# Kernel optimization log

Measured on AMD Instinct MI355X. Metric: run time of the kernel, lower is better.

Reference implementation:

```python
import jax, jax.numpy as jnp
import numpy as np

EMBED = 1024
HEADS = 16
HEAD_DIM = EMBED // HEADS


def setup_inputs() -> dict:
    key = jax.random.key(0)
    ks = jax.random.split(key, 9)
    B, S = 1, 4096
    scale = 1.0 / np.sqrt(EMBED)
    x = jax.random.normal(ks[0], (B, S, EMBED), dtype=jnp.float32)
    # nn.Linear weights stored as [out, in]; we store transposed [in, out] for x @ W
    Wq = jax.random.uniform(ks[1], (EMBED, EMBED), jnp.float32, -scale, scale)
    bq = jax.random.uniform(ks[2], (EMBED,), jnp.float32, -scale, scale)
    Wk = jax.random.uniform(ks[3], (EMBED, EMBED), jnp.float32, -scale, scale)
    bk = jax.random.uniform(ks[4], (EMBED,), jnp.float32, -scale, scale)
    Wv = jax.random.uniform(ks[5], (EMBED, EMBED), jnp.float32, -scale, scale)
    bv = jax.random.uniform(ks[6], (EMBED,), jnp.float32, -scale, scale)
    Wo = jax.random.uniform(ks[7], (EMBED, EMBED), jnp.float32, -scale, scale)
    bo = jax.random.uniform(ks[8], (EMBED,), jnp.float32, -scale, scale)
    return {"x": x, "Wq": Wq, "bq": bq, "Wk": Wk, "bk": bk,
            "Wv": Wv, "bv": bv, "Wo": Wo, "bo": bo}


def reference(x, Wq, bq, Wk, bk, Wv, bv, Wo, bo):
    B, S, E = x.shape
    H, D = HEADS, HEAD_DIM
    # projections
    Q = (x @ Wq + bq).reshape(B, S, H, D).transpose(0, 2, 1, 3)  # [B,H,S,D]
    K = (x @ Wk + bk).reshape(B, S, H, D).transpose(0, 2, 1, 3)
    V = (x @ Wv + bv).reshape(B, S, H, D).transpose(0, 2, 1, 3)
    # unfused attention: full [B,H,S,S] score matrix, matching the torch module
    scores = jnp.einsum('bhqd,bhkd->bhqk', Q, K) / jnp.sqrt(jnp.float32(D)).astype(x.dtype)
    probs = jax.nn.softmax(scores, axis=-1)
    out = jnp.einsum('bhqk,bhkd->bhqd', probs, V)  # [B,H,S,D]
    out = out.transpose(0, 2, 1, 3).reshape(B, S, E)
    return out @ Wo + bo
```

## Files before the change

### kernel.cpp

```cpp
#include <hip/hip_runtime.h>


constexpr int Sq = 4096;
constexpr int Ee = 1024;
constexpr int Hh = 16;
constexpr int Dh = 64;

typedef _Float16 half8 __attribute__((ext_vector_type(8)));
typedef _Float16 half4 __attribute__((ext_vector_type(4)));
typedef _Float16 half2t __attribute__((ext_vector_type(2)));
typedef float f32x4 __attribute__((ext_vector_type(4)));

union U8 { half8 v8; half2t h2[4]; };

__device__ __forceinline__ unsigned short f2h(float f) {
  _Float16 h = (_Float16)f;
  return *reinterpret_cast<unsigned short*>(&h);
}

__device__ __forceinline__ half2t pk(float a, float b) {
  return __builtin_bit_cast(half2t, __builtin_amdgcn_cvt_pkrtz(a, b));
}

__device__ __forceinline__ void gload16(const void* g, void* l) {
  __builtin_amdgcn_global_load_lds(
      (const __attribute__((address_space(1))) void*)g,
      (__attribute__((address_space(3))) void*)l, 16, 0, 0);
}

__global__ void k_prep(const float* __restrict__ x,
                       const float* __restrict__ Wq, const float* __restrict__ Wk,
                       const float* __restrict__ Wv, const float* __restrict__ Wo,
                       unsigned short* __restrict__ xb,
                       unsigned short* __restrict__ Wqt, unsigned short* __restrict__ Wkt,
                       unsigned short* __restrict__ Wvt, unsigned short* __restrict__ Wot) {
  int b = blockIdx.x, t = threadIdx.x;
  if (b < 4096) {
    int i = b * 256 + t;
    float4 v = reinterpret_cast<const float4*>(x)[i];
    ushort4 o;
    o.x = f2h(v.x); o.y = f2h(v.y); o.z = f2h(v.z); o.w = f2h(v.w);
    reinterpret_cast<ushort4*>(xb)[i] = o;
    return;
  }
  __shared__ unsigned short tile[64][65];
  int r = b - 4096;
  int wi = r >> 8, ti = r & 255;
  const float* W = (wi == 0) ? Wq : (wi == 1) ? Wk : (wi == 2) ? Wv : Wo;
  unsigned short* Wt = (wi == 0) ? Wqt : (wi == 1) ? Wkt : (wi == 2) ? Wvt : Wot;
  int kb = (ti & 15) * 64, nb = (ti >> 4) * 64;
  int r0 = t >> 4, c4 = (t & 15) * 4;
  for (int i = 0; i < 4; i++) {
    int row = r0 + i * 16;
    float4 v = *reinterpret_cast<const float4*>(W + (size_t)(kb + row) * Ee + nb + c4);
    tile[row][c4 + 0] = f2h(v.x); tile[row][c4 + 1] = f2h(v.y);
    tile[row][c4 + 2] = f2h(v.z); tile[row][c4 + 3] = f2h(v.w);
  }
  __syncthreads();
  for (int i = 0; i < 4; i++) {
    int nrow = r0 + i * 16;
    ushort4 o;
    o.x = tile[c4 + 0][nrow]; o.y = tile[c4 + 1][nrow];
    o.z = tile[c4 + 2][nrow]; o.w = tile[c4 + 3][nrow];
    *reinterpret_cast<ushort4*>(Wt + (size_t)(nb + nrow) * Ee + kb + c4) = o;
  }
}

template <bool TR>
__device__ __forceinline__ void gemm_kloop(
    const unsigned short* __restrict__ A, const unsigned short* __restrict__ Wt,
    unsigned short* Al, unsigned short* Bl,
    int m0, int n0, int t, int wm, int wn, int quad, int c, f32x4 (&acc)[4][4]) {
  for (int k0 = 0; k0 < 1024; k0 += 64) {
    __syncthreads();
#pragma unroll
    for (int i = 0; i < 4; i++) {
      int ch = i * 256 + t;
      int row = ch >> 3, kg = (ch & 7) ^ (row & 7);
      gload16(A + (size_t)(m0 + row) * 1024 + k0 + kg * 8, &Al[ch * 8]);
    }
#pragma unroll
    for (int i = 0; i < 4; i++) {
      int ch = i * 256 + t;
      int row = ch >> 3, kg = (ch & 7) ^ (row & 7);
      gload16(Wt + (size_t)(n0 + row) * 1024 + k0 + kg * 8, &Bl[ch * 8]);
    }
    __syncthreads();
#pragma unroll
    for (int ks = 0; ks < 2; ks++) {
      half8 af[4], bfr[4];
#pragma unroll
      for (int i = 0; i < 4; i++) {
        int row = wm * 64 + i * 16 + c;
        int kg = (quad + 4 * ks) ^ (row & 7);
        af[i] = *reinterpret_cast<const half8*>(&Al[row * 64 + kg * 8]);
      }
#pragma unroll
      for (int j = 0; j < 4; j++) {
        int row = wn * 64 + j * 16 + c;
        int kg = (quad + 4 * ks) ^ (row & 7);
        bfr[j] = *reinterpret_cast<const half8*>(&Bl[row * 64 + kg * 8]);
      }
#pragma unroll
      for (int i = 0; i < 4; i++)
#pragma unroll
        for (int j = 0; j < 4; j++) {
          if (TR)
            acc[j][i] = __builtin_amdgcn_mfma_f32_16x16x32_f16(bfr[j], af[i], acc[j][i], 0, 0, 0);
          else
            acc[i][j] = __builtin_amdgcn_mfma_f32_16x16x32_f16(af[i], bfr[j], acc[i][j], 0, 0, 0);
        }
    }
  }
}

__global__ __launch_bounds__(256) void k_gemm(
    const unsigned short* __restrict__ A,
    const unsigned short* __restrict__ W0, const unsigned short* __restrict__ W1,
    const unsigned short* __restrict__ W2,
    const float* __restrict__ b0, const float* __restrict__ b1, const float* __restrict__ b2,
    void* d0, void* d1, void* d2) {
  __shared__ __align__(16) unsigned short Al[128 * 64];
  __shared__ __align__(16) unsigned short Bl[128 * 64];
  const unsigned short* Wt; const float* bias; void* dst;
  if (blockIdx.z == 0)      { Wt = W0; bias = b0; dst = d0; }
  else if (blockIdx.z == 1) { Wt = W1; bias = b1; dst = d1; }
  else                      { Wt = W2; bias = b2; dst = d2; }

  int t = threadIdx.x;
  int w = t >> 6, L = t & 63, quad = L >> 4, c = L & 15;
  int m0 = blockIdx.x * 128, n0 = blockIdx.y * 128;
  int wm = w >> 1, wn = w & 1;

  f32x4 zero = {0.f, 0.f, 0.f, 0.f};
  f32x4 acc[4][4];
#pragma unroll
  for (int i = 0; i < 4; i++)
#pragma unroll
    for (int j = 0; j < 4; j++) acc[i][j] = zero;

  if (blockIdx.z < 2) gemm_kloop<true>(A, Wt, Al, Bl, m0, n0, t, wm, wn, quad, c, acc);
  else                gemm_kloop<false>(A, Wt, Al, Bl, m0, n0, t, wm, wn, quad, c, acc);

  if (blockIdx.z < 2) {
    float sc = (blockIdx.z == 0) ? 0.18033688011112042f : 1.0f;
    unsigned short* qk = (unsigned short*)dst;
#pragma unroll
    for (int j = 0; j < 4; j++) {
      int nb4 = n0 + wn * 64 + j * 16 + quad * 4;
      int hh = nb4 >> 6, d = nb4 & 63;
      f32x4 b4 = *reinterpret_cast<const f32x4*>(bias + nb4);
#pragma unroll
      for (int i = 0; i < 4; i++) {
        int s = m0 + wm * 64 + i * 16 + c;
        half4 hv;
#pragma unroll
        for (int r = 0; r < 4; r++) hv[r] = (_Float16)((acc[j][i][r] + b4[r]) * sc);
        *reinterpret_cast<half4*>(&qk[(size_t)hh * Sq * Dh + (size_t)s * Dh + d]) = hv;
      }
    }
    return;
  }
  unsigned short* Vt = (unsigned short*)dst;
#pragma unroll
  for (int j = 0; j < 4; j++) {
    int n = n0 + wn * 64 + j * 16 + c;
    int hh = n >> 6, d = n & 63;
    float bv = bias[n];
#pragma unroll
    for (int i = 0; i < 4; i++) {
      int pos = m0 + wm * 64 + (i >> 1) * 32 + quad * 8 + (i & 1) * 4;
      half4 hv;
#pragma unroll
      for (int r = 0; r < 4; r++) hv[r] = (_Float16)(acc[i][j][r] + bv);
      *reinterpret_cast<half4*>(&Vt[(size_t)hh * Dh * Sq + (size_t)d * Sq + pos]) = hv;
    }
  }
}

__global__ __launch_bounds__(256) void k_gemmO(
    const unsigned short* __restrict__ A, const unsigned short* __restrict__ Wt,
    const float* __restrict__ bias, float* __restrict__ out) {
  __shared__ __align__(16) unsigned short Al[64 * 64];
  __shared__ __align__(16) unsigned short Bl[128 * 64];
  int t = threadIdx.x;
  int w = t >> 6, L = t & 63, quad = L >> 4, c = L & 15;
  int m0 = blockIdx.x * 64, n0 = blockIdx.y * 128;
  int wm = w & 1, wn = w >> 1;

  f32x4 zero = {0.f, 0.f, 0.f, 0.f};
  f32x4 acc[4][2];
#pragma unroll
  for (int j = 0; j < 4; j++)
#pragma unroll
    for (int i = 0; i < 2; i++) acc[j][i] = zero;

  for (int k0 = 0; k0 < 1024; k0 += 64) {
    __syncthreads();
#pragma unroll
    for (int i = 0; i < 2; i++) {
      int ch = i * 256 + t;
      int row = ch >> 3, kg = (ch & 7) ^ (row & 7);
      gload16(A + (size_t)(m0 + row) * 1024 + k0 + kg * 8, &Al[ch * 8]);
    }
#pragma unroll
    for (int i = 0; i < 4; i++) {
      int ch = i * 256 + t;
      int row = ch >> 3, kg = (ch & 7) ^ (row & 7);
      gload16(Wt + (size_t)(n0 + row) * 1024 + k0 + kg * 8, &Bl[ch * 8]);
    }
    __syncthreads();
#pragma unroll
    for (int ks = 0; ks < 2; ks++) {
      half8 af[2], bfr[4];
#pragma unroll
      for (int i = 0; i < 2; i++) {
        int row = wm * 32 + i * 16 + c;
        int kg = (quad + 4 * ks) ^ (row & 7);
        af[i] = *reinterpret_cast<const half8*>(&Al[row * 64 + kg * 8]);
      }
#pragma unroll
      for (int j = 0; j < 4; j++) {
        int row = wn * 64 + j * 16 + c;
        int kg = (quad + 4 * ks) ^ (row & 7);
        bfr[j] = *reinterpret_cast<const half8*>(&Bl[row * 64 + kg * 8]);
      }
#pragma unroll
      for (int j = 0; j < 4; j++)
#pragma unroll
        for (int i = 0; i < 2; i++)
          acc[j][i] = __builtin_amdgcn_mfma_f32_16x16x32_f16(bfr[j], af[i], acc[j][i], 0, 0, 0);
    }
  }

#pragma unroll
  for (int j = 0; j < 4; j++) {
    int nb4 = n0 + wn * 64 + j * 16 + quad * 4;
    f32x4 b4 = *reinterpret_cast<const f32x4*>(bias + nb4);
#pragma unroll
    for (int i = 0; i < 2; i++) {
      int s = m0 + wm * 32 + i * 16 + c;
      f32x4 v = acc[j][i] + b4;
      *reinterpret_cast<f32x4*>(out + (size_t)s * 1024 + nb4) = v;
    }
  }
}

__global__ __launch_bounds__(512, 4) void k_attn(
    const unsigned short* __restrict__ Q, const unsigned short* __restrict__ K,
    const unsigned short* __restrict__ Vt, unsigned short* __restrict__ O) {
  __shared__ __align__(16) unsigned short SM[32768];
  int t = threadIdx.x;
  int w = t >> 6, L = t & 63, quad = L >> 4, c = L & 15;
  int wl = w & 3, par = w >> 2;
  int h = blockIdx.y, qb = blockIdx.x;
  const unsigned short* Qh = Q + (size_t)h * Sq * Dh;
  const unsigned short* Kh = K + (size_t)h * Sq * Dh;
  const unsigned short* Vth = Vt + (size_t)h * Dh * Sq;

  half8 qf[2][2];
#pragma unroll
  for (int qg = 0; qg < 2; qg++) {
    int qrow = qb * 128 + wl * 32 + qg * 16 + c;
#pragma unroll
    for (int ks = 0; ks < 2; ks++)
      qf[qg][ks] = *reinterpret_cast<const half8*>(Qh + (size_t)qrow * Dh + ks * 32 + quad * 8);
  }

  f32x4 zero = {0.f, 0.f, 0.f, 0.f};
  f32x4 o0[4], o1[4];
#pragma unroll
  for (int i = 0; i < 4; i++) { o0[i] = zero; o1[i] = zero; }
  f32x4 l0 = zero, l1 = zero;
  half8 ones8;
#pragma unroll
  for (int j = 0; j < 8; j++) ones8[j] = (_Float16)1.0f;

  int koff[2][4], voff[4][2];
#pragma unroll
  for (int ks = 0; ks < 2; ks++)
#pragma unroll
    for (int nt = 0; nt < 4; nt++) {
      int row = nt * 16 + c;
      koff[ks][nt] = par * 4096 + row * 64 + (((ks * 4 + quad) ^ (row & 7)) * 8);
    }
#pragma unroll
  for (int dt = 0; dt < 4; dt++)
#pragma unroll
    for (int n2 = 0; n2 < 2; n2++) {
      int row = dt * 16 + c;
      voff[dt][n2] = (2 + par) * 4096 + row * 64 + (((n2 * 4 + quad) ^ (row & 7)) * 8);
    }

  int srow = t >> 3, skg = (t & 7) ^ (srow & 7);
  const unsigned short* Kg = Kh + srow * Dh + skg * 8;
  const unsigned short* Vg = Vth + (size_t)srow * Sq + skg * 8;

#pragma unroll
  for (int p2 = 0; p2 < 2; p2++) {
    gload16(Kg + p2 * 4096, &SM[p2 * 4096 + t * 8]);
    gload16(Vg + p2 * 64, &SM[(2 + p2) * 4096 + t * 8]);
  }

  auto body = [&](int BUFOFF) {
    f32x4 st0[4], st1[4];
#pragma unroll
    for (int nt = 0; nt < 4; nt++) { st0[nt] = zero; st1[nt] = zero; }
#pragma unroll
    for (int ks = 0; ks < 2; ks++)
#pragma unroll
      for (int nt = 0; nt < 4; nt++) {
        half8 kfv = *reinterpret_cast<const half8*>(&SM[koff[ks][nt] + BUFOFF]);
        st0[nt] = __builtin_amdgcn_mfma_f32_16x16x32_f16(kfv, qf[0][ks], st0[nt], 0, 0, 0);
        st1[nt] = __builtin_amdgcn_mfma_f32_16x16x32_f16(kfv, qf[1][ks], st1[nt], 0, 0, 0);
      }
    half8 pB0[2], pB1[2];
#pragma unroll
    for (int n2 = 0; n2 < 2; n2++) {
      U8 u;
      u.h2[0] = pk(__builtin_amdgcn_exp2f(st0[2 * n2][0]), __builtin_amdgcn_exp2f(st0[2 * n2][1]));
      u.h2[1] = pk(__builtin_amdgcn_exp2f(st0[2 * n2][2]), __builtin_amdgcn_exp2f(st0[2 * n2][3]));
      u.h2[2] = pk(__builtin_amdgcn_exp2f(st0[2 * n2 + 1][0]), __builtin_amdgcn_exp2f(st0[2 * n2 + 1][1]));
      u.h2[3] = pk(__builtin_amdgcn_exp2f(st0[2 * n2 + 1][2]), __builtin_amdgcn_exp2f(st0[2 * n2 + 1][3]));
      pB0[n2] = u.v8;
      U8 v;
      v.h2[0] = pk(__builtin_amdgcn_exp2f(st1[2 * n2][0]), __builtin_amdgcn_exp2f(st1[2 * n2][1]));
      v.h2[1] = pk(__builtin_amdgcn_exp2f(st1[2 * n2][2]), __builtin_amdgcn_exp2f(st1[2 * n2][3]));
      v.h2[2] = pk(__builtin_amdgcn_exp2f(st1[2 * n2 + 1][0]), __builtin_amdgcn_exp2f(st1[2 * n2 + 1][1]));
      v.h2[3] = pk(__builtin_amdgcn_exp2f(st1[2 * n2 + 1][2]), __builtin_amdgcn_exp2f(st1[2 * n2 + 1][3]));
      pB1[n2] = v.v8;
      l0 = __builtin_amdgcn_mfma_f32_16x16x32_f16(ones8, pB0[n2], l0, 0, 0, 0);
      l1 = __builtin_amdgcn_mfma_f32_16x16x32_f16(ones8, pB1[n2], l1, 0, 0, 0);
    }
#pragma unroll
    for (int dt = 0; dt < 4; dt++)
#pragma unroll
      for (int n2 = 0; n2 < 2; n2++) {
        half8 vv = *reinterpret_cast<const half8*>(&SM[voff[dt][n2] + BUFOFF]);
        o0[dt] = __builtin_amdgcn_mfma_f32_16x16x32_f16(vv, pB0[n2], o0[dt], 0, 0, 0);
        o1[dt] = __builtin_amdgcn_mfma_f32_16x16x32_f16(vv, pB1[n2], o1[dt], 0, 0, 0);
      }
  };

  for (int ob2 = 0; ob2 < 16; ob2++) {
    __syncthreads();
    {
      int tb = 4 * ob2 + 2;
#pragma unroll
      for (int p2 = 0; p2 < 2; p2++) {
        gload16(Kg + (size_t)(tb + p2) * 4096, &SM[16384 + p2 * 4096 + t * 8]);
        gload16(Vg + (tb + p2) * 64, &SM[16384 + (2 + p2) * 4096 + t * 8]);
      }
    }
    body(0);
    __syncthreads();
    if (ob2 < 15) {
      int tb = 4 * ob2 + 4;
#pragma unroll
      for (int p2 = 0; p2 < 2; p2++) {
        gload16(Kg + (size_t)(tb + p2) * 4096, &SM[p2 * 4096 + t * 8]);
        gload16(Vg + (tb + p2) * 64, &SM[(2 + p2) * 4096 + t * 8]);
      }
    }
    body(16384);
  }

  __syncthreads();
  float* cb = (float*)SM;
  if (par == 1) {
#pragma unroll
    for (int v = 0; v < 4; v++) {
      *reinterpret_cast<f32x4*>(cb + ((wl * 9 + v) * 64 + L) * 4) = o0[v];
      *reinterpret_cast<f32x4*>(cb + ((wl * 9 + 4 + v) * 64 + L) * 4) = o1[v];
    }
    f32x4 lv = {l0[0], l1[0], 0.f, 0.f};
    *reinterpret_cast<f32x4*>(cb + ((wl * 9 + 8) * 64 + L) * 4) = lv;
  }
  __syncthreads();
  if (par == 0) {
#pragma unroll
    for (int v = 0; v < 4; v++) {
      o0[v] += *reinterpret_cast<const f32x4*>(cb + ((wl * 9 + v) * 64 + L) * 4);
      o1[v] += *reinterpret_cast<const f32x4*>(cb + ((wl * 9 + 4 + v) * 64 + L) * 4);
    }
    f32x4 lv = *reinterpret_cast<const f32x4*>(cb + ((wl * 9 + 8) * 64 + L) * 4);
    float lt0 = l0[0] + lv[0], lt1 = l1[0] + lv[1];

#pragma unroll
    for (int qg = 0; qg < 2; qg++) {
      float inv = 1.f / (qg ? lt1 : lt0);
      f32x4* oo = qg ? o1 : o0;
      int q = qb * 128 + wl * 32 + qg * 16 + c;
#pragma unroll
      for (int dt = 0; dt < 4; dt++) {
        half4 hv;
#pragma unroll
        for (int r = 0; r < 4; r++) hv[r] = (_Float16)(oo[dt][r] * inv);
        *reinterpret_cast<half4*>(&O[(size_t)q * 1024 + h * 64 + dt * 16 + quad * 4]) = hv;
      }
    }
  }
}

extern "C" void kernel_launch(void* const* d_in, const int* in_sizes, int n_in,
                              void* d_out, int out_size, void* d_ws, size_t ws_size,
                              hipStream_t stream) {
  const float* x  = (const float*)d_in[0];
  const float* Wq = (const float*)d_in[1];
  const float* bq = (const float*)d_in[2];
  const float* Wk = (const float*)d_in[3];
  const float* bk = (const float*)d_in[4];
  const float* Wv = (const float*)d_in[5];
  const float* bv = (const float*)d_in[6];
  const float* Wo = (const float*)d_in[7];
  const float* bo = (const float*)d_in[8];

  char* ws = (char*)d_ws;
  const size_t MB = 1u << 20;
  unsigned short* xb  = (unsigned short*)(ws);
  unsigned short* Wqt = (unsigned short*)(ws + 8 * MB);
  unsigned short* Wkt = (unsigned short*)(ws + 10 * MB);
  unsigned short* Wvt = (unsigned short*)(ws + 12 * MB);
  unsigned short* Wot = (unsigned short*)(ws + 14 * MB);
  unsigned short* Qb  = (unsigned short*)(ws + 16 * MB);
  unsigned short* Kb  = (unsigned short*)(ws + 24 * MB);
  unsigned short* Vtg = (unsigned short*)(ws + 32 * MB);
  unsigned short* Ob  = (unsigned short*)(ws + 40 * MB);

  k_prep<<<5120, 256, 0, stream>>>(x, Wq, Wk, Wv, Wo, xb, Wqt, Wkt, Wvt, Wot);
  k_gemm<<<dim3(32, 8, 3), 256, 0, stream>>>(xb, Wqt, Wkt, Wvt, bq, bk, bv,
                                             (void*)Qb, (void*)Kb, (void*)Vtg);
  k_attn<<<dim3(32, 16), 512, 0, stream>>>(Qb, Kb, Vtg, Ob);
  k_gemmO<<<dim3(64, 8), 256, 0, stream>>>(Ob, Wot, bo, (float*)d_out);
}
```

Baseline: 226.9 us.

## Halve attention block to 4 waves, each handling 64 query rows

The attention kernel now uses 256 threads (4 waves) per block instead of 512. Each wave processes 64 query rows rather than 32, so every K/V fragment read from LDS is reused across four query groups. The cooperative K/V staging loop is doubled per thread, and s_setprio hints are placed around the MFMA phases. The intent is to cut LDS read traffic per FLOP and improve MFMA density, at the cost of more registers per wave (more accumulators) and fewer waves to hide latency.

After: 219.9 us. 1.03x faster.

```diff
diff --git a/kernel.cpp b/kernel.cpp
--- a/kernel.cpp
+++ b/kernel.cpp
@@ -246,32 +246,36 @@
   }
 }
 
-__global__ __launch_bounds__(512, 4) void k_attn(
+__global__ __launch_bounds__(256, 2) void k_attn(
     const unsigned short* __restrict__ Q, const unsigned short* __restrict__ K,
     const unsigned short* __restrict__ Vt, unsigned short* __restrict__ O) {
   __shared__ __align__(16) unsigned short SM[32768];
   int t = threadIdx.x;
   int w = t >> 6, L = t & 63, quad = L >> 4, c = L & 15;
-  int wl = w & 3, par = w >> 2;
+  int wl = w & 1, par = w >> 1;
   int h = blockIdx.y, qb = blockIdx.x;
   const unsigned short* Qh = Q + (size_t)h * Sq * Dh;
   const unsigned short* Kh = K + (size_t)h * Sq * Dh;
   const unsigned short* Vth = Vt + (size_t)h * Dh * Sq;
 
-  half8 qf[2][2];
-#pragma unroll
-  for (int qg = 0; qg < 2; qg++) {
-    int qrow = qb * 128 + wl * 32 + qg * 16 + c;
+  half8 qf[4][2];
+#pragma unroll
+  for (int qg = 0; qg < 4; qg++) {
+    int qrow = qb * 128 + wl * 64 + qg * 16 + c;
 #pragma unroll
     for (int ks = 0; ks < 2; ks++)
       qf[qg][ks] = *reinterpret_cast<const half8*>(Qh + (size_t)qrow * Dh + ks * 32 + quad * 8);
   }
 
   f32x4 zero = {0.f, 0.f, 0.f, 0.f};
-  f32x4 o0[4], o1[4];
-#pragma unroll
-  for (int i = 0; i < 4; i++) { o0[i] = zero; o1[i] = zero; }
-  f32x4 l0 = zero, l1 = zero;
+  f32x4 o[4][4];
+  f32x4 l[4];
+#pragma unroll
+  for (int qg = 0; qg < 4; qg++) {
+    l[qg] = zero;
+#pragma unroll
+    for (int dt = 0; dt < 4; dt++) o[qg][dt] = zero;
+  }
   half8 ones8;
 #pragma unroll
   for (int j = 0; j < 8; j++) ones8[j] = (_Float16)1.0f;
@@ -292,76 +296,82 @@
       voff[dt][n2] = (2 + par) * 4096 + row * 64 + (((n2 * 4 + quad) ^ (row & 7)) * 8);
     }
 
-  int srow = t >> 3, skg = (t & 7) ^ (srow & 7);
-  const unsigned short* Kg = Kh + srow * Dh + skg * 8;
-  const unsigned short* Vg = Vth + (size_t)srow * Sq + skg * 8;
-
-#pragma unroll
-  for (int p2 = 0; p2 < 2; p2++) {
-    gload16(Kg + p2 * 4096, &SM[p2 * 4096 + t * 8]);
-    gload16(Vg + p2 * 64, &SM[(2 + p2) * 4096 + t * 8]);
-  }
+  const unsigned short* KgB[2];
+  const unsigned short* VgB[2];
+#pragma unroll
+  for (int i = 0; i < 2; i++) {
+    int ch = i * 256 + t;
+    int row = ch >> 3, kg = (ch & 7) ^ (row & 7);
+    KgB[i] = Kh + row * Dh + kg * 8;
+    VgB[i] = Vth + (size_t)row * Sq + kg * 8;
+  }
+
+  auto stage = [&](int bufo, int tb) {
+#pragma unroll
+    for (int p2 = 0; p2 < 2; p2++) {
+#pragma unroll
+      for (int i = 0; i < 2; i++)
+        gload16(KgB[i] + (size_t)(tb + p2) * 4096, &SM[bufo + p2 * 4096 + (i * 256 + t) * 8]);
+#pragma unroll
+      for (int i = 0; i < 2; i++)
+        gload16(VgB[i] + (size_t)(tb + p2) * 64, &SM[bufo + (2 + p2) * 4096 + (i * 256 + t) * 8]);
+    }
+  };
+
+  stage(0, 0);
 
   auto body = [&](int BUFOFF) {
-    f32x4 st0[4], st1[4];
-#pragma unroll
-    for (int nt = 0; nt < 4; nt++) { st0[nt] = zero; st1[nt] = zero; }
-#pragma unroll
-    for (int ks = 0; ks < 2; ks++)
-#pragma unroll
-      for (int nt = 0; nt < 4; nt++) {
-        half8 kfv = *reinterpret_cast<const half8*>(&SM[koff[ks][nt] + BUFOFF]);
-        st0[nt] = __builtin_amdgcn_mfma_f32_16x16x32_f16(kfv, qf[0][ks], st0[nt], 0, 0, 0);
-        st1[nt] = __builtin_amdgcn_mfma_f32_16x16x32_f16(kfv, qf[1][ks], st1[nt], 0, 0, 0);
-      }
-    half8 pB0[2], pB1[2];
-#pragma unroll
-    for (int n2 = 0; n2 < 2; n2++) {
-      U8 u;
-      u.h2[0] = pk(__builtin_amdgcn_exp2f(st0[2 * n2][0]), __builtin_amdgcn_exp2f(st0[2 * n2][1]));
-      u.h2[1] = pk(__builtin_amdgcn_exp2f(st0[2 * n2][2]), __builtin_amdgcn_exp2f(st0[2 * n2][3]));
-      u.h2[2] = pk(__builtin_amdgcn_exp2f(st0[2 * n2 + 1][0]), __builtin_amdgcn_exp2f(st0[2 * n2 + 1][1]));
-      u.h2[3] = pk(__builtin_amdgcn_exp2f(st0[2 * n2 + 1][2]), __builtin_amdgcn_exp2f(st0[2 * n2 + 1][3]));
-      pB0[n2] = u.v8;
-      U8 v;
-      v.h2[0] = pk(__builtin_amdgcn_exp2f(st1[2 * n2][0]), __builtin_amdgcn_exp2f(st1[2 * n2][1]));
-      v.h2[1] = pk(__builtin_amdgcn_exp2f(st1[2 * n2][2]), __builtin_amdgcn_exp2f(st1[2 * n2][3]));
-      v.h2[2] = pk(__builtin_amdgcn_exp2f(st1[2 * n2 + 1][0]), __builtin_amdgcn_exp2f(st1[2 * n2 + 1][1]));
-      v.h2[3] = pk(__builtin_amdgcn_exp2f(st1[2 * n2 + 1][2]), __builtin_amdgcn_exp2f(st1[2 * n2 + 1][3]));
-      pB1[n2] = v.v8;
-      l0 = __builtin_amdgcn_mfma_f32_16x16x32_f16(ones8, pB0[n2], l0, 0, 0, 0);
-      l1 = __builtin_amdgcn_mfma_f32_16x16x32_f16(ones8, pB1[n2], l1, 0, 0, 0);
-    }
+    half8 pB[4][2];
+#pragma unroll
+    for (int h2 = 0; h2 < 2; h2++) {
+      f32x4 st[2][4];
+#pragma unroll
+      for (int q2 = 0; q2 < 2; q2++)
+#pragma unroll
+        for (int nt = 0; nt < 4; nt++) st[q2][nt] = zero;
+      __builtin_amdgcn_s_setprio(1);
+#pragma unroll
+      for (int ks = 0; ks < 2; ks++)
+#pragma unroll
+        for (int nt = 0; nt < 4; nt++) {
+          half8 kfv = *reinterpret_cast<const half8*>(&SM[koff[ks][nt] + BUFOFF]);
+          st[0][nt] = __builtin_amdgcn_mfma_f32_16x16x32_f16(kfv, qf[2 * h2 + 0][ks], st[0][nt], 0, 0, 0);
+          st[1][nt] = __builtin_amdgcn_mfma_f32_16x16x32_f16(kfv, qf[2 * h2 + 1][ks], st[1][nt], 0, 0, 0);
+        }
+      __builtin_amdgcn_s_setprio(0);
+#pragma unroll
+      for (int q2 = 0; q2 < 2; q2++)
+#pragma unroll
+        for (int n2 = 0; n2 < 2; n2++) {
+          U8 u;
+          u.h2[0] = pk(__builtin_amdgcn_exp2f(st[q2][2 * n2][0]), __builtin_amdgcn_exp2f(st[q2][2 * n2][1]));
+          u.h2[1] = pk(__builtin_amdgcn_exp2f(st[q2][2 * n2][2]), __builtin_amdgcn_exp2f(st[q2][2 * n2][3]));
+          u.h2[2] = pk(__builtin_amdgcn_exp2f(st[q2][2 * n2 + 1][0]), __builtin_amdgcn_exp2f(st[q2][2 * n2 + 1][1]));
+          u.h2[3] = pk(__builtin_amdgcn_exp2f(st[q2][2 * n2 + 1][2]), __builtin_amdgcn_exp2f(st[q2][2 * n2 + 1][3]));
+          pB[2 * h2 + q2][n2] = u.v8;
+          l[2 * h2 + q2] = __builtin_amdgcn_mfma_f32_16x16x32_f16(ones8, u.v8, l[2 * h2 + q2], 0, 0, 0);
+        }
+    }
+    __builtin_amdgcn_s_setprio(1);
 #pragma unroll
     for (int dt = 0; dt < 4; dt++)
 #pragma unroll
       for (int n2 = 0; n2 < 2; n2++) {
         half8 vv = *reinterpret_cast<const half8*>(&SM[voff[dt][n2] + BUFOFF]);
-        o0[dt] = __builtin_amdgcn_mfma_f32_16x16x32_f16(vv, pB0[n2], o0[dt], 0, 0, 0);
-        o1[dt] = __builtin_amdgcn_mfma_f32_16x16x32_f16(vv, pB1[n2], o1[dt], 0, 0, 0);
-      }
+        o[0][dt] = __builtin_amdgcn_mfma_f32_16x16x32_f16(vv, pB[0][n2], o[0][dt], 0, 0, 0);
+        o[1][dt] = __builtin_amdgcn_mfma_f32_16x16x32_f16(vv, pB[1][n2], o[1][dt], 0, 0, 0);
+        o[2][dt] = __builtin_amdgcn_mfma_f32_16x16x32_f16(vv, pB[2][n2], o[2][dt], 0, 0, 0);
+        o[3][dt] = __builtin_amdgcn_mfma_f32_16x16x32_f16(vv, pB[3][n2], o[3][dt], 0, 0, 0);
+      }
+    __builtin_amdgcn_s_setprio(0);
   };
 
   for (int ob2 = 0; ob2 < 16; ob2++) {
     __syncthreads();
-    {
-      int tb = 4 * ob2 + 2;
-#pragma unroll
-      for (int p2 = 0; p2 < 2; p2++) {
-        gload16(Kg + (size_t)(tb + p2) * 4096, &SM[16384 + p2 * 4096 + t * 8]);
-        gload16(Vg + (tb + p2) * 64, &SM[16384 + (2 + p2) * 4096 + t * 8]);
-      }
-    }
+    stage(16384, 4 * ob2 + 2);
     body(0);
     __syncthreads();
-    if (ob2 < 15) {
-      int tb = 4 * ob2 + 4;
-#pragma unroll
-      for (int p2 = 0; p2 < 2; p2++) {
-        gload16(Kg + (size_t)(tb + p2) * 4096, &SM[p2 * 4096 + t * 8]);
-        gload16(Vg + (tb + p2) * 64, &SM[(2 + p2) * 4096 + t * 8]);
-      }
-    }
+    if (ob2 < 15) stage(0, 4 * ob2 + 4);
     body(16384);
   }
 
@@ -369,33 +379,30 @@
   float* cb = (float*)SM;
   if (par == 1) {
 #pragma unroll
-    for (int v = 0; v < 4; v++) {
-      *reinterpret_cast<f32x4*>(cb + ((wl * 9 + v) * 64 + L) * 4) = o0[v];
-      *reinterpret_cast<f32x4*>(cb + ((wl * 9 + 4 + v) * 64 + L) * 4) = o1[v];
-    }
-    f32x4 lv = {l0[0], l1[0], 0.f, 0.f};
-    *reinterpret_cast<f32x4*>(cb + ((wl * 9 + 8) * 64 + L) * 4) = lv;
+    for (int qg = 0; qg < 4; qg++)
+#pragma unroll
+      for (int dt = 0; dt < 4; dt++)
+        *reinterpret_cast<f32x4*>(cb + ((wl * 17 + qg * 4 + dt) * 64 + L) * 4) = o[qg][dt];
+    f32x4 lv = {l[0][0], l[1][0], l[2][0], l[3][0]};
+    *reinterpret_cast<f32x4*>(cb + ((wl * 17 + 16) * 64 + L) * 4) = lv;
   }
   __syncthreads();
   if (par == 0) {
 #pragma unroll
-    for (int v = 0; v < 4; v++) {
-      o0[v] += *reinterpret_cast<const f32x4*>(cb + ((wl * 9 + v) * 64 + L) * 4);
-      o1[v] += *reinterpret_cast<const f32x4*>(cb + ((wl * 9 + 4 + v) * 64 + L) * 4);
-    }
-    f32x4 lv = *reinterpret_cast<const f32x4*>(cb + ((wl * 9 + 8) * 64 + L) * 4);
-    float lt0 = l0[0] + lv[0], lt1 = l1[0] + lv[1];
-
-#pragma unroll
-    for (int qg = 0; qg < 2; qg++) {
-      float inv = 1.f / (qg ? lt1 : lt0);
-      f32x4* oo = qg ? o1 : o0;
-      int q = qb * 128 + wl * 32 + qg * 16 + c;
+    for (int qg = 0; qg < 4; qg++)
+#pragma unroll
+      for (int dt = 0; dt < 4; dt++)
+        o[qg][dt] += *reinterpret_cast<const f32x4*>(cb + ((wl * 17 + qg * 4 + dt) * 64 + L) * 4);
+    f32x4 lv = *reinterpret_cast<const f32x4*>(cb + ((wl * 17 + 16) * 64 + L) * 4);
+#pragma unroll
+    for (int qg = 0; qg < 4; qg++) {
+      float inv = 1.f / (l[qg][0] + lv[qg]);
+      int q = qb * 128 + wl * 64 + qg * 16 + c;
 #pragma unroll
       for (int dt = 0; dt < 4; dt++) {
         half4 hv;
 #pragma unroll
-        for (int r = 0; r < 4; r++) hv[r] = (_Float16)(oo[dt][r] * inv);
+        for (int r = 0; r < 4; r++) hv[r] = (_Float16)(o[qg][dt][r] * inv);
         *reinterpret_cast<half4*>(&O[(size_t)q * 1024 + h * 64 + dt * 16 + quad * 4]) = hv;
       }
     }
@@ -430,6 +437,6 @@
   k_prep<<<5120, 256, 0, stream>>>(x, Wq, Wk, Wv, Wo, xb, Wqt, Wkt, Wvt, Wot);
   k_gemm<<<dim3(32, 8, 3), 256, 0, stream>>>(xb, Wqt, Wkt, Wvt, bq, bk, bv,
                                              (void*)Qb, (void*)Kb, (void*)Vtg);
-  k_attn<<<dim3(32, 16), 512, 0, stream>>>(Qb, Kb, Vtg, Ob);
+  k_attn<<<dim3(32, 16), 256, 0, stream>>>(Qb, Kb, Vtg, Ob);
   k_gemmO<<<dim3(64, 8), 256, 0, stream>>>(Ob, Wot, bo, (float*)d_out);
 }
```
